# Performance work log

Measured on AMD Instinct MI355X. Metric: run time of the kernel, lower is better.

## Reference

```python
import jax, jax.numpy as jnp
import numpy as np

B, L, D_MODEL = 2, 2048, 1024
N_HEADS, D_K = 16, 64  # d_v == d_k (required by the output*q epilogue)


def setup_inputs() -> dict:
    key = jax.random.key(0)
    ks = jax.random.split(key, 8)
    # xavier_normal std for [d_model, d_k] fan: sqrt(2/(d_model+d_k))
    std = float(np.sqrt(2.0 / (D_MODEL + D_K)))
    std_p = float(np.sqrt(1.0 / (N_HEADS * D_K)))  # nn.Linear default ~ U(-1/sqrt(fan_in),..); normal approx ok for a baseline
    return {
        "q": jax.random.normal(ks[0], (B, L, D_MODEL), jnp.float32),
        "k": jax.random.normal(ks[1], (B, L, D_MODEL), jnp.float32),
        "v": jax.random.normal(ks[2], (B, L, D_MODEL), jnp.float32),
        "w_qs": jax.random.normal(ks[3], (N_HEADS, D_MODEL, D_K), jnp.float32) * std,
        "w_ks": jax.random.normal(ks[4], (N_HEADS, D_MODEL, D_K), jnp.float32) * std,
        "w_vs": jax.random.normal(ks[5], (N_HEADS, D_MODEL, D_K), jnp.float32) * std,
        "w_proj": jax.random.normal(ks[6], (D_MODEL, N_HEADS * D_K), jnp.float32) * std_p,
        "b_proj": jnp.zeros((D_MODEL,), jnp.float32),
    }


def reference(q, k, v, w_qs, w_ks, w_vs, w_proj, b_proj):
    # Per-head projections: [h, B, L, d_k]
    qh = jnp.einsum("bld,hdk->hblk", q, w_qs)
    kh = jnp.einsum("bld,hdk->hblk", k, w_ks)
    vh = jnp.einsum("bld,hdk->hblk", v, w_vs)
    # UNscaled attention (no 1/sqrt(d_k)), dropout is identity at eval
    attn = jax.nn.softmax(jnp.einsum("hblk,hbmk->hblm", qh, kh), axis=-1)
    # attn @ V with elementwise *q epilogue
    out = jnp.einsum("hblm,hbmk->hblk", attn, vh) * qh
    # torch.cat(torch.split(outputs, mb_size, 0), -1): heads concat on last dim
    out = out.transpose(1, 2, 0, 3).reshape(q.shape[0], q.shape[1], -1)  # [B, L, h*d_k]
    return out @ w_proj.T + b_proj
```

## Files before the change

### kernel.cpp

```cpp
#include <hip/hip_runtime.h>

#define B_ 2
#define L_ 2048
#define DM 1024
#define H_ 16
#define DK 64
#define ROWS (B_*L_)
#define BK 32
#define LDT 40

typedef _Float16 f16x8 __attribute__((ext_vector_type(8)));
typedef float    f32x4 __attribute__((ext_vector_type(4)));
typedef unsigned short us8 __attribute__((ext_vector_type(8)));
typedef unsigned short us4v __attribute__((ext_vector_type(4)));

__device__ __forceinline__ unsigned short f2h(float f) {
    _Float16 h = (_Float16)f;
    return __builtin_bit_cast(unsigned short, h);
}
__device__ __forceinline__ float h2f(unsigned short u) {
    return (float)__builtin_bit_cast(_Float16, u);
}
__device__ __forceinline__ f16x8 ld8h(const unsigned short* p) {
    return *reinterpret_cast<const f16x8*>(p);
}
__device__ __forceinline__ us8 cvt_us8(float4 a, float4 b) {
    us8 u;
    u[0] = f2h(a.x); u[1] = f2h(a.y); u[2] = f2h(a.z); u[3] = f2h(a.w);
    u[4] = f2h(b.x); u[5] = f2h(b.y); u[6] = f2h(b.z); u[7] = f2h(b.w);
    return u;
}

#define MFMA(a, b, c) __builtin_amdgcn_mfma_f32_16x16x32_f16((a), (b), (c), 0, 0, 0)

#define AS1 __attribute__((address_space(1)))
#define AS3 __attribute__((address_space(3)))
__device__ __forceinline__ void glds16(const void* g, void* l) {
    __builtin_amdgcn_global_load_lds((const AS1 unsigned int*)g,
                                     (AS3 unsigned int*)l, 16, 0, 0);
}

__global__ __launch_bounds__(256) void kcvt(
    const float* __restrict__ src, unsigned short* __restrict__ dst)
{
    size_t i = ((size_t)blockIdx.x * 256 + threadIdx.x) * 8;
    const float4* s4 = (const float4*)(src + i);
    *(us8*)(dst + i) = cvt_us8(s4[0], s4[1]);
}

__global__ __launch_bounds__(256) void kcvt3(
    const float* __restrict__ q, const float* __restrict__ k,
    const float* __restrict__ v, unsigned short* __restrict__ dst)
{
    int bx = blockIdx.x;
    int which = bx >> 11, rem = bx & 2047;
    const float* src = (which == 0) ? q : (which == 1) ? k : v;
    size_t i = ((size_t)rem * 256 + threadIdx.x) * 8;
    const float4* s4 = (const float4*)(src + i);
    *(us8*)(dst + (size_t)which * ROWS * DM + i) = cvt_us8(s4[0], s4[1]);
}

__global__ __launch_bounds__(256) void k0_transpose_w(
    const float* __restrict__ wq,
    const float* __restrict__ wk,
    const float* __restrict__ wv,
    unsigned short* __restrict__ wt)
{
    __shared__ unsigned short tile[64][65];
    int bx = blockIdx.x;
    int which = bx / (H_ * 16);
    int rem   = bx % (H_ * 16);
    int h  = rem >> 4;
    int db = (rem & 15) * 64;
    const float* src = (which == 0) ? wq : (which == 1) ? wk : wv;
    float scale = (which == 1) ? 1.44269504f : 1.0f;

    int t = threadIdx.x;
    int r = t >> 2;
    int c = (t & 3) * 16;
    const float4* sp = (const float4*)(src + ((size_t)(h * DM + db + r)) * DK + c);
    #pragma unroll
    for (int i4 = 0; i4 < 4; i4++) {
        float4 f = sp[i4];
        tile[r][c + i4 * 4 + 0] = f2h(f.x * scale);
        tile[r][c + i4 * 4 + 1] = f2h(f.y * scale);
        tile[r][c + i4 * 4 + 2] = f2h(f.z * scale);
        tile[r][c + i4 * 4 + 3] = f2h(f.w * scale);
    }
    __syncthreads();

    int n   = t >> 2;
    int d16 = (t & 3) * 16;
    __align__(16) unsigned short ov[16];
    #pragma unroll
    for (int i = 0; i < 16; i++) ov[i] = tile[d16 + i][n];
    size_t off = (((size_t)which * H_ + h) * DK + n) * DM + db + d16;
    *(us8*)(wt + off)     = *(us8*)&ov[0];
    *(us8*)(wt + off + 8) = *(us8*)&ov[8];
}

__global__ __launch_bounds__(256) void k1_proj_fp16(
    const unsigned short* __restrict__ qkvh,
    const unsigned short* __restrict__ wt,
    unsigned short* __restrict__ qh,
    unsigned short* __restrict__ kh,
    unsigned short* __restrict__ vt)
{
    __shared__ __align__(16) unsigned short sA[128 * BK];
    __shared__ __align__(16) unsigned short sB[128 * BK];

    int bx = blockIdx.x;
    int which = bx >> 8;
    int rem   = bx & 255;
    int mbase = (rem >> 3) * 128;
    int nbase = (rem & 7) * 128;

    const unsigned short* Ag = qkvh + (size_t)which * ROWS * DM;
    const unsigned short* Bg = wt + (size_t)which * DM * DM;

    int t = threadIdx.x;
    int wave = t >> 6, lane = t & 63, quad = lane >> 4, l16 = lane & 15;
    int wm = (wave >> 1) * 64, wn = (wave & 1) * 64;

    const unsigned short* gA0 = Ag + (size_t)(mbase + (t >> 2)) * DM + (t & 3) * 8;
    const unsigned short* gA1 = gA0 + (size_t)64 * DM;
    const unsigned short* gB0 = Bg + (size_t)(nbase + (t >> 2)) * DM + (t & 3) * 8;
    const unsigned short* gB1 = gB0 + (size_t)64 * DM;
    unsigned short* lA0 = &sA[(size_t)t * 8];
    unsigned short* lA1 = &sA[(size_t)(256 + t) * 8];
    unsigned short* lB0 = &sB[(size_t)t * 8];
    unsigned short* lB1 = &sB[(size_t)(256 + t) * 8];

    f32x4 acc[4][4];
    #pragma unroll
    for (int mi = 0; mi < 4; mi++)
        #pragma unroll
        for (int ni = 0; ni < 4; ni++) acc[mi][ni] = (f32x4)0.0f;

    for (int step = 0; step < 32; step++) {
        if (step) __syncthreads();
        glds16(gA0, lA0); glds16(gA1, lA1);
        glds16(gB0, lB0); glds16(gB1, lB1);
        gA0 += BK; gA1 += BK; gB0 += BK; gB1 += BK;
        __syncthreads();

        f16x8 aF[4], bF[4];
        #pragma unroll
        for (int mi = 0; mi < 4; mi++)
            aF[mi] = *(const f16x8*)&sA[(wm + mi * 16 + l16) * BK + quad * 8];
        #pragma unroll
        for (int ni = 0; ni < 4; ni++)
            bF[ni] = *(const f16x8*)&sB[(wn + ni * 16 + l16) * BK + quad * 8];
        __builtin_amdgcn_s_setprio(1);
        #pragma unroll
        for (int mi = 0; mi < 4; mi++)
            #pragma unroll
            for (int ni = 0; ni < 4; ni++)
                acc[mi][ni] = MFMA(aF[mi], bF[ni], acc[mi][ni]);
        __builtin_amdgcn_s_setprio(0);
    }

    int h = (nbase >> 6) + (wave & 1);
    if (which < 2) {
        unsigned short* OUT = ((which == 0) ? qh : kh) + (size_t)h * ROWS * DK;
        #pragma unroll
        for (int mi = 0; mi < 4; mi++)
            #pragma unroll
            for (int ni = 0; ni < 4; ni++)
                #pragma unroll
                for (int r = 0; r < 4; r++) {
                    int row = mbase + wm + mi * 16 + quad * 4 + r;
                    OUT[(size_t)row * DK + ni * 16 + l16] = f2h(acc[mi][ni][r]);
                }
    } else {
        unsigned short* OUT = vt + (size_t)h * DK * ROWS;
        #pragma unroll
        for (int mi = 0; mi < 4; mi++)
            #pragma unroll
            for (int ni = 0; ni < 4; ni++) {
                int dk   = ni * 16 + l16;
                int rowb = mbase + wm + mi * 16 + quad * 4;
                us4v pk;
                pk[0] = f2h(acc[mi][ni][0]); pk[1] = f2h(acc[mi][ni][1]);
                pk[2] = f2h(acc[mi][ni][2]); pk[3] = f2h(acc[mi][ni][3]);
                *(us4v*)(OUT + (size_t)dk * ROWS + rowb) = pk;
            }
    }
}

__global__ __launch_bounds__(256) void k1_proj_qkv(
    const float* __restrict__ q,
    const float* __restrict__ k,
    const float* __restrict__ v,
    const unsigned short* __restrict__ wt,
    unsigned short* __restrict__ qh,
    unsigned short* __restrict__ kh,
    unsigned short* __restrict__ vt)
{
    __shared__ __align__(16) unsigned short sA[128 * LDT];
    __shared__ __align__(16) unsigned short sB[128 * LDT];

    int bx = blockIdx.x;
    int which = bx >> 8;
    int rem   = bx & 255;
    int mbase = (rem >> 3) * 128;
    int nbase = (rem & 7) * 128;

    const float* Ag = (which == 0) ? q : (which == 1) ? k : v;
    const unsigned short* Bg = wt + (size_t)which * DM * DM;

    int t = threadIdx.x;
    int wave = t >> 6, lane = t & 63, quad = lane >> 4, l16 = lane & 15;
    int wm = (wave >> 1) * 64, wn = (wave & 1) * 64;

    int ar0 = t >> 2,         ac0 = t & 3;
    int ar1 = (256 + t) >> 2, ac1 = t & 3;
    const float* pA0 = Ag + (size_t)(mbase + ar0) * DM + ac0 * 8;
    const float* pA1 = Ag + (size_t)(mbase + ar1) * DM + ac1 * 8;
    const unsigned short* pB0 = Bg + (size_t)(nbase + ar0) * DM + ac0 * 8;
    const unsigned short* pB1 = Bg + (size_t)(nbase + ar1) * DM + ac1 * 8;
    unsigned short* wA0 = &sA[ar0 * LDT + ac0 * 8];
    unsigned short* wA1 = &sA[ar1 * LDT + ac1 * 8];
    unsigned short* wB0 = &sB[ar0 * LDT + ac0 * 8];
    unsigned short* wB1 = &sB[ar1 * LDT + ac1 * 8];

    f32x4 acc[4][4];
    #pragma unroll
    for (int mi = 0; mi < 4; mi++)
        #pragma unroll
        for (int ni = 0; ni < 4; ni++) acc[mi][ni] = (f32x4)0.0f;

    float4 rA0a = *(const float4*)pA0, rA0b = *(const float4*)(pA0 + 4);
    float4 rA1a = *(const float4*)pA1, rA1b = *(const float4*)(pA1 + 4);
    us8 rB0 = *(const us8*)pB0, rB1 = *(const us8*)pB1;

    for (int step = 0; step < 32; step++) {
        if (step) __syncthreads();
        *(us8*)wA0 = cvt_us8(rA0a, rA0b);
        *(us8*)wA1 = cvt_us8(rA1a, rA1b);
        *(us8*)wB0 = rB0; *(us8*)wB1 = rB1;
        __syncthreads();
        if (step < 31) {
            pA0 += BK; pA1 += BK; pB0 += BK; pB1 += BK;
            rA0a = *(const float4*)pA0; rA0b = *(const float4*)(pA0 + 4);
            rA1a = *(const float4*)pA1; rA1b = *(const float4*)(pA1 + 4);
            rB0 = *(const us8*)pB0; rB1 = *(const us8*)pB1;
        }
        f16x8 aF[4], bF[4];
        #pragma unroll
        for (int mi = 0; mi < 4; mi++)
            aF[mi] = *(const f16x8*)&sA[(wm + mi * 16 + l16) * LDT + quad * 8];
        #pragma unroll
        for (int ni = 0; ni < 4; ni++)
            bF[ni] = *(const f16x8*)&sB[(wn + ni * 16 + l16) * LDT + quad * 8];
        #pragma unroll
        for (int mi = 0; mi < 4; mi++)
            #pragma unroll
            for (int ni = 0; ni < 4; ni++)
                acc[mi][ni] = MFMA(aF[mi], bF[ni], acc[mi][ni]);
    }

    int h = (nbase >> 6) + (wave & 1);
    if (which < 2) {
        unsigned short* OUT = ((which == 0) ? qh : kh) + (size_t)h * ROWS * DK;
        #pragma unroll
        for (int mi = 0; mi < 4; mi++)
            #pragma unroll
            for (int ni = 0; ni < 4; ni++)
                #pragma unroll
                for (int r = 0; r < 4; r++) {
                    int row = mbase + wm + mi * 16 + quad * 4 + r;
                    OUT[(size_t)row * DK + ni * 16 + l16] = f2h(acc[mi][ni][r]);
                }
    } else {
        unsigned short* OUT = vt + (size_t)h * DK * ROWS;
        #pragma unroll
        for (int mi = 0; mi < 4; mi++)
            #pragma unroll
            for (int ni = 0; ni < 4; ni++) {
                int dk   = ni * 16 + l16;
                int rowb = mbase + wm + mi * 16 + quad * 4;
                us4v pk;
                pk[0] = f2h(acc[mi][ni][0]); pk[1] = f2h(acc[mi][ni][1]);
                pk[2] = f2h(acc[mi][ni][2]); pk[3] = f2h(acc[mi][ni][3]);
                *(us4v*)(OUT + (size_t)dk * ROWS + rowb) = pk;
            }
    }
}

__global__ __launch_bounds__(256) void k2_attn(
    const unsigned short* __restrict__ qh,
    const unsigned short* __restrict__ kh,
    const unsigned short* __restrict__ vt,
    unsigned short* __restrict__ x2)
{
    __shared__ __align__(16) unsigned short ktile[2][64][64];
    __shared__ __align__(16) unsigned short vtile[2][64][64];
    __shared__ __align__(16) unsigned short pld[4][16][64];

    int bx = blockIdx.x;
    int xcd = bx & 7;
    int loc = bx >> 3;
    int hb  = xcd * 4 + (loc >> 5);
    int qt  = loc & 31;
    int h = hb >> 1, b = hb & 1;
    int qbase = qt * 64;

    const unsigned short* qhp = qh + ((size_t)h * ROWS + b * L_) * DK;
    const unsigned short* khp = kh + ((size_t)h * ROWS + b * L_) * DK;
    const unsigned short* vtp = vt + (size_t)h * DK * ROWS + b * L_;

    int wave = threadIdx.x >> 6, lane = threadIdx.x & 63;
    int quad = lane >> 4, l16 = lane & 15;
    int t = threadIdx.x;
    int g8 = (l16 & 7) * 8;

    int c0 = t,       key0 = c0 >> 3, ss0 = ((c0 & 7) ^ (key0 & 7)) * 8;
    int c1 = 256 + t, key1 = c1 >> 3, ss1 = ((c1 & 7) ^ (key1 & 7)) * 8;
    const unsigned short* kg0 = khp + (size_t)key0 * DK + ss0;
    const unsigned short* kg1 = khp + (size_t)key1 * DK + ss1;
    const unsigned short* vg0 = vtp + (size_t)key0 * ROWS + ss0;
    const unsigned short* vg1 = vtp + (size_t)key1 * ROWS + ss1;
    unsigned short* kl0[2] = { &ktile[0][0][0] + c0 * 8, &ktile[1][0][0] + c0 * 8 };
    unsigned short* kl1[2] = { &ktile[0][0][0] + c1 * 8, &ktile[1][0][0] + c1 * 8 };
    unsigned short* vl0[2] = { &vtile[0][0][0] + c0 * 8, &vtile[1][0][0] + c0 * 8 };
    unsigned short* vl1[2] = { &vtile[0][0][0] + c1 * 8, &vtile[1][0][0] + c1 * 8 };

    const unsigned short* kgp0 = kg0 + (size_t)2 * 64 * DK;
    const unsigned short* kgp1 = kg1 + (size_t)2 * 64 * DK;
    const unsigned short* vgp0 = vg0 + 64;
    const unsigned short* vgp1 = vg1 + 64;

    glds16(kg0, kl0[0]); glds16(kg1, kl1[0]);
    glds16(kg0 + (size_t)64 * DK, kl0[1]); glds16(kg1 + (size_t)64 * DK, kl1[1]);
    glds16(vg0, vl0[0]); glds16(vg1, vl1[0]);

    int qrow = qbase + wave * 16 + l16;
    f16x8 qb0 = ld8h(qhp + (size_t)qrow * DK + quad * 8);
    f16x8 qb1 = ld8h(qhp + (size_t)qrow * DK + 32 + quad * 8);

    float m_i = -1e30f, l_i = 0.0f;
    f32x4 o[4];
    #pragma unroll
    for (int nt = 0; nt < 4; nt++) o[nt] = (f32x4)0.0f;

    f32x4 s0[4], s1[4];

    __syncthreads();

    #pragma unroll
    for (int nt = 0; nt < 4; nt++) s0[nt] = (f32x4)0.0f;
    __builtin_amdgcn_s_setprio(1);
    #pragma unroll
    for (int nt = 0; nt < 4; nt++) {
        const unsigned short* kr = &ktile[0][nt * 16 + l16][0];
        f16x8 ka0 = *(const f16x8*)(kr + ((quad * 8) ^ g8));
        f16x8 ka1 = *(const f16x8*)(kr + ((32 + quad * 8) ^ g8));
        s0[nt] = MFMA(ka0, qb0, s0[nt]);
        s0[nt] = MFMA(ka1, qb1, s0[nt]);
    }
    __builtin_amdgcn_s_setprio(0);
    __syncthreads();

#define K2_BODY(SP, SN, KT, CUR)                                              \
    {                                                                         \
        if ((KT) < 31) {                                                      \
            _Pragma("unroll")                                                 \
            for (int nt = 0; nt < 4; nt++) SN[nt] = (f32x4)0.0f;              \
            __builtin_amdgcn_s_setprio(1);                                    \
            _Pragma("unroll")                                                 \
            for (int nt = 0; nt < 4; nt++) {                                  \
                const unsigned short* kr = &ktile[(CUR)^1][nt * 16 + l16][0]; \
                f16x8 ka0 = *(const f16x8*)(kr + ((quad * 8) ^ g8));          \
                f16x8 ka1 = *(const f16x8*)(kr + ((32 + quad * 8) ^ g8));     \
                SN[nt] = MFMA(ka0, qb0, SN[nt]);                              \
                SN[nt] = MFMA(ka1, qb1, SN[nt]);                              \
            }                                                                 \
            __builtin_amdgcn_s_setprio(0);                                    \
        }                                                                     \
        if ((KT) < 30) {                                                      \
            glds16(kgp0, kl0[CUR]); glds16(kgp1, kl1[CUR]);                   \
            kgp0 += (size_t)64 * DK; kgp1 += (size_t)64 * DK;                 \
        }                                                                     \
        if ((KT) < 31) {                                                      \
            glds16(vgp0, vl0[(CUR)^1]); glds16(vgp1, vl1[(CUR)^1]);           \
            vgp0 += 64; vgp1 += 64;                                           \
        }                                                                     \
                                                 \
        float pm[4];                                                          \
        _Pragma("unroll")                                                     \
        for (int nt = 0; nt < 4; nt++) {                                      \
            float a = fmaxf(SP[nt][0], SP[nt][1]);                            \
            float c2 = fmaxf(SP[nt][2], SP[nt][3]);                           \
            pm[nt] = fmaxf(a, c2);                                            \
        }                                                                     \
        float mx = fmaxf(fmaxf(pm[0], pm[1]), fmaxf(pm[2], pm[3]));           \
        mx = fmaxf(mx, __shfl_xor(mx, 16));                                   \
        mx = fmaxf(mx, __shfl_xor(mx, 32));                                   \
        if (!__all(mx - m_i <= 11.0f)) {                                      \
            float mnew  = fmaxf(m_i, mx);                                     \
            float alpha = __builtin_amdgcn_exp2f(m_i - mnew);                 \
            l_i *= alpha;                                                     \
            _Pragma("unroll")                                                 \
            for (int r = 0; r < 4; r++) {                                     \
                float av = __shfl(alpha, quad * 4 + r);                       \
                _Pragma("unroll")                                             \
                for (int nt = 0; nt < 4; nt++) o[nt][r] *= av;                \
            }                                                                 \
            m_i = mnew;                                                       \
        }                                                                     \
        float ps[4];                                                          \
        _Pragma("unroll")                                                     \
        for (int nt = 0; nt < 4; nt++) {                                      \
            float e0 = __builtin_amdgcn_exp2f(SP[nt][0] - m_i);               \
            float e1 = __builtin_amdgcn_exp2f(SP[nt][1] - m_i);               \
            float e2 = __builtin_amdgcn_exp2f(SP[nt][2] - m_i);               \
            float e3 = __builtin_amdgcn_exp2f(SP[nt][3] - m_i);               \
            SP[nt][0] = e0; SP[nt][1] = e1; SP[nt][2] = e2; SP[nt][3] = e3;   \
            ps[nt] = (e0 + e1) + (e2 + e3);                                   \
        }                                                                     \
        float rs = (ps[0] + ps[1]) + (ps[2] + ps[3]);                         \
        rs += __shfl_xor(rs, 16);                                             \
        rs += __shfl_xor(rs, 32);                                             \
        l_i += rs;                                                            \
        _Pragma("unroll")                                                     \
        for (int nt = 0; nt < 4; nt++) {                                      \
            us4v pk;                                                          \
            pk[0] = f2h(SP[nt][0]); pk[1] = f2h(SP[nt][1]);                   \
            pk[2] = f2h(SP[nt][2]); pk[3] = f2h(SP[nt][3]);                   \
            *(us4v*)&pld[wave][l16][(nt * 16 + quad * 4) ^ g8] = pk;          \
        }                                                                     \
                                                      \
        __builtin_amdgcn_s_setprio(1);                                        \
        _Pragma("unroll")                                                     \
        for (int kk = 0; kk < 2; kk++) {                                      \
            f16x8 pa = *(const f16x8*)&pld[wave][l16][(kk*32 + quad*8) ^ g8]; \
            _Pragma("unroll")                                                 \
            for (int nt = 0; nt < 4; nt++) {                                  \
                const unsigned short* vr = &vtile[CUR][nt * 16 + l16][0];     \
                f16x8 vb = *(const f16x8*)(vr + ((kk * 32 + quad * 8) ^ g8)); \
                o[nt] = MFMA(pa, vb, o[nt]);                                  \
            }                                                                 \
        }                                                                     \
        __builtin_amdgcn_s_setprio(0);                                        \
        __syncthreads();                                                      \
    }

    for (int kt = 0; kt < 32; kt += 2) {
        K2_BODY(s0, s1, kt,     0)
        K2_BODY(s1, s0, kt + 1, 1)
    }
#undef K2_BODY

    float linv = 1.0f / l_i;
    #pragma unroll
    for (int r = 0; r < 4; r++) {
        float lv = __shfl(linv, quad * 4 + r);
        int row = qbase + wave * 16 + quad * 4 + r;
        #pragma unroll
        for (int nt = 0; nt < 4; nt++) {
            int col = nt * 16 + l16;
            float qv = h2f(qhp[(size_t)row * DK + col]);
            float val = o[nt][r] * lv * qv;
            x2[((size_t)b * L_ + row) * DM + h * DK + col] = f2h(val);
        }
    }
}

__global__ __launch_bounds__(256) void k3_out_proj(
    const unsigned short* __restrict__ x2,
    const unsigned short* __restrict__ wph,
    const float* __restrict__ bias,
    float* __restrict__ out)
{
    __shared__ __align__(16) unsigned short sA[128 * BK];
    __shared__ __align__(16) unsigned short sB[128 * BK];

    int bx = blockIdx.x;
    int mbase = (bx >> 3) * 128;
    int nbase = (bx & 7) * 128;

    int t = threadIdx.x;
    int wave = t >> 6, lane = t & 63, quad = lane >> 4, l16 = lane & 15;
    int wm = (wave >> 1) * 64, wn = (wave & 1) * 64;

    const unsigned short* gA0 = x2 + (size_t)(mbase + (t >> 2)) * DM + (t & 3) * 8;
    const unsigned short* gA1 = gA0 + (size_t)64 * DM;
    const unsigned short* gB0 = wph + (size_t)(nbase + (t >> 2)) * DM + (t & 3) * 8;
    const unsigned short* gB1 = gB0 + (size_t)64 * DM;
    unsigned short* lA0 = &sA[(size_t)t * 8];
    unsigned short* lA1 = &sA[(size_t)(256 + t) * 8];
    unsigned short* lB0 = &sB[(size_t)t * 8];
    unsigned short* lB1 = &sB[(size_t)(256 + t) * 8];

    f32x4 acc[4][4];
    #pragma unroll
    for (int mi = 0; mi < 4; mi++)
        #pragma unroll
        for (int ni = 0; ni < 4; ni++) acc[mi][ni] = (f32x4)0.0f;

    for (int step = 0; step < 32; step++) {
        if (step) __syncthreads();
        glds16(gA0, lA0); glds16(gA1, lA1);
        glds16(gB0, lB0); glds16(gB1, lB1);
        gA0 += BK; gA1 += BK; gB0 += BK; gB1 += BK;
        __syncthreads();

        f16x8 aF[4], bF[4];
        #pragma unroll
        for (int mi = 0; mi < 4; mi++)
            aF[mi] = *(const f16x8*)&sA[(wm + mi * 16 + l16) * BK + quad * 8];
        #pragma unroll
        for (int ni = 0; ni < 4; ni++)
            bF[ni] = *(const f16x8*)&sB[(wn + ni * 16 + l16) * BK + quad * 8];
        __builtin_amdgcn_s_setprio(1);
        #pragma unroll
        for (int mi = 0; mi < 4; mi++)
            #pragma unroll
            for (int ni = 0; ni < 4; ni++)
                acc[mi][ni] = MFMA(aF[mi], bF[ni], acc[mi][ni]);
        __builtin_amdgcn_s_setprio(0);
    }

    float bv[4];
    #pragma unroll
    for (int ni = 0; ni < 4; ni++) bv[ni] = bias[nbase + wn + ni * 16 + l16];

    #pragma unroll
    for (int mi = 0; mi < 4; mi++)
        #pragma unroll
        for (int ni = 0; ni < 4; ni++)
            #pragma unroll
            for (int r = 0; r < 4; r++) {
                int row = mbase + wm + mi * 16 + quad * 4 + r;
                int col = nbase + wn + ni * 16 + l16;
                out[(size_t)row * DM + col] = acc[mi][ni][r] + bv[ni];
            }
}

extern "C" void kernel_launch(void* const* d_in, const int* in_sizes, int n_in,
                              void* d_out, int out_size, void* d_ws, size_t ws_size,
                              hipStream_t stream)
{
    const float* q     = (const float*)d_in[0];
    const float* k     = (const float*)d_in[1];
    const float* v     = (const float*)d_in[2];
    const float* wqs   = (const float*)d_in[3];
    const float* wks   = (const float*)d_in[4];
    const float* wvs   = (const float*)d_in[5];
    const float* wproj = (const float*)d_in[6];
    const float* bproj = (const float*)d_in[7];
    float* out = (float*)d_out;

    char* ws = (char*)d_ws;
    #define MB (size_t)(1024 * 1024)
    unsigned short* wt   = (unsigned short*)(ws);
    unsigned short* wph  = (unsigned short*)(ws + 6  * MB);
    unsigned short* qh   = (unsigned short*)(ws + 8  * MB);
    unsigned short* kh   = (unsigned short*)(ws + 16 * MB);
    unsigned short* vt   = (unsigned short*)(ws + 24 * MB);
    unsigned short* x2   = (unsigned short*)(ws + 32 * MB);
    unsigned short* qkvh = (unsigned short*)(ws + 32 * MB);

    kcvt<<<dim3((DM * DM) / (256 * 8)), dim3(256), 0, stream>>>(wproj, wph);
    k0_transpose_w<<<dim3(3 * H_ * 16), dim3(256), 0, stream>>>(wqs, wks, wvs, wt);

    if (ws_size >= 56 * MB) {
        kcvt3<<<dim3(3 * 2048), dim3(256), 0, stream>>>(q, k, v, qkvh);
        k1_proj_fp16<<<dim3(3 * 32 * 8), dim3(256), 0, stream>>>(qkvh, wt, qh, kh, vt);
    } else {
        k1_proj_qkv<<<dim3(3 * 32 * 8), dim3(256), 0, stream>>>(q, k, v, wt, qh, kh, vt);
    }
    k2_attn<<<dim3(H_ * B_ * 32), dim3(256), 0, stream>>>(qh, kh, vt, x2);
    k3_out_proj<<<dim3(32 * 8), dim3(256), 0, stream>>>(x2, wph, bproj, out);
}
```

Before: 254.8 us.

## Fuse fp32 input conversion into projection GEMM, swizzle LDS, restructure attention pipeline

Removes the separate fp32-to-fp16 conversion pass over q, k, v and has the projection GEMM load fp32 tiles into LDS directly via global_load_lds, converting to fp16 when it reads the fragments. This saves a full read and write of the activations, at the cost of twice the LDS traffic and conversion work inside the loop. Both GEMMs also get XOR-swizzled LDS layouts to avoid bank conflicts and a block-index remap for better L2 locality. The attention loop changes from computing the next tile's scores ahead to a simpler single-step double buffer, and switches to packed cvt_pkrtz for P.

```diff
diff --git a/kernel.cpp b/kernel.cpp
--- a/kernel.cpp
+++ b/kernel.cpp
@@ -7,9 +7,10 @@
 #define DK 64
 #define ROWS (B_*L_)
 #define BK 32
-#define LDT 40
 
 typedef _Float16 f16x8 __attribute__((ext_vector_type(8)));
+typedef __fp16   fp16v2 __attribute__((ext_vector_type(2)));
+typedef __fp16   fp16v4 __attribute__((ext_vector_type(4)));
 typedef float    f32x4 __attribute__((ext_vector_type(4)));
 typedef unsigned short us8 __attribute__((ext_vector_type(8)));
 typedef unsigned short us4v __attribute__((ext_vector_type(4)));
@@ -46,18 +47,6 @@
     size_t i = ((size_t)blockIdx.x * 256 + threadIdx.x) * 8;
     const float4* s4 = (const float4*)(src + i);
     *(us8*)(dst + i) = cvt_us8(s4[0], s4[1]);
-}
-
-__global__ __launch_bounds__(256) void kcvt3(
-    const float* __restrict__ q, const float* __restrict__ k,
-    const float* __restrict__ v, unsigned short* __restrict__ dst)
-{
-    int bx = blockIdx.x;
-    int which = bx >> 11, rem = bx & 2047;
-    const float* src = (which == 0) ? q : (which == 1) ? k : v;
-    size_t i = ((size_t)rem * 256 + threadIdx.x) * 8;
-    const float4* s4 = (const float4*)(src + i);
-    *(us8*)(dst + (size_t)which * ROWS * DM + i) = cvt_us8(s4[0], s4[1]);
 }
 
 __global__ __launch_bounds__(256) void k0_transpose_w(
@@ -99,37 +88,50 @@
     *(us8*)(wt + off + 8) = *(us8*)&ov[8];
 }
 
-__global__ __launch_bounds__(256) void k1_proj_fp16(
-    const unsigned short* __restrict__ qkvh,
+__global__ __launch_bounds__(256) void k1_proj(
+    const float* __restrict__ q,
+    const float* __restrict__ k,
+    const float* __restrict__ v,
     const unsigned short* __restrict__ wt,
     unsigned short* __restrict__ qh,
     unsigned short* __restrict__ kh,
     unsigned short* __restrict__ vt)
 {
-    __shared__ __align__(16) unsigned short sA[128 * BK];
-    __shared__ __align__(16) unsigned short sB[128 * BK];
-
-    int bx = blockIdx.x;
+    __shared__ __align__(16) float          sAf[128 * 32];
+    __shared__ __align__(16) unsigned short sB [128 * 32];
+
+    int bxr = blockIdx.x;
+    int bx  = (bxr & 7) * 96 + (bxr >> 3);
     int which = bx >> 8;
     int rem   = bx & 255;
     int mbase = (rem >> 3) * 128;
     int nbase = (rem & 7) * 128;
 
-    const unsigned short* Ag = qkvh + (size_t)which * ROWS * DM;
+    const float* Ag = (which == 0) ? q : (which == 1) ? k : v;
     const unsigned short* Bg = wt + (size_t)which * DM * DM;
 
     int t = threadIdx.x;
     int wave = t >> 6, lane = t & 63, quad = lane >> 4, l16 = lane & 15;
     int wm = (wave >> 1) * 64, wn = (wave & 1) * 64;
-
-    const unsigned short* gA0 = Ag + (size_t)(mbase + (t >> 2)) * DM + (t & 3) * 8;
-    const unsigned short* gA1 = gA0 + (size_t)64 * DM;
-    const unsigned short* gB0 = Bg + (size_t)(nbase + (t >> 2)) * DM + (t & 3) * 8;
-    const unsigned short* gB1 = gB0 + (size_t)64 * DM;
-    unsigned short* lA0 = &sA[(size_t)t * 8];
-    unsigned short* lA1 = &sA[(size_t)(256 + t) * 8];
-    unsigned short* lB0 = &sB[(size_t)t * 8];
-    unsigned short* lB1 = &sB[(size_t)(256 + t) * 8];
+    int xa = l16 & 7;
+    int xb = (l16 >> 1) & 3;
+
+    const float* gA[4]; float* lA[4];
+    #pragma unroll
+    for (int i = 0; i < 4; i++) {
+        int c = i * 256 + t;
+        int row = c >> 3, sl = (c & 7) ^ (row & 7);
+        gA[i] = Ag + (size_t)(mbase + row) * DM + sl * 4;
+        lA[i] = sAf + c * 4;
+    }
+    const unsigned short* gB[2]; unsigned short* lB[2];
+    #pragma unroll
+    for (int i = 0; i < 2; i++) {
+        int c = i * 256 + t;
+        int row = c >> 2, sl = (c & 3) ^ ((row >> 1) & 3);
+        gB[i] = Bg + (size_t)(nbase + row) * DM + sl * 8;
+        lB[i] = sB + c * 8;
+    }
 
     f32x4 acc[4][4];
     #pragma unroll
@@ -139,18 +141,31 @@
 
     for (int step = 0; step < 32; step++) {
         if (step) __syncthreads();
-        glds16(gA0, lA0); glds16(gA1, lA1);
-        glds16(gB0, lB0); glds16(gB1, lB1);
-        gA0 += BK; gA1 += BK; gB0 += BK; gB1 += BK;
+        glds16(gA[0], lA[0]); glds16(gA[1], lA[1]);
+        glds16(gA[2], lA[2]); glds16(gA[3], lA[3]);
+        glds16(gB[0], lB[0]); glds16(gB[1], lB[1]);
+        #pragma unroll
+        for (int i = 0; i < 4; i++) gA[i] += BK;
+        gB[0] += BK; gB[1] += BK;
         __syncthreads();
 
         f16x8 aF[4], bF[4];
         #pragma unroll
-        for (int mi = 0; mi < 4; mi++)
-            aF[mi] = *(const f16x8*)&sA[(wm + mi * 16 + l16) * BK + quad * 8];
+        for (int mi = 0; mi < 4; mi++) {
+            const float* ar = sAf + (wm + mi * 16 + l16) * 32;
+            f32x4 a0 = *(const f32x4*)(ar + (((quad * 2)     ^ xa) * 4));
+            f32x4 a1 = *(const f32x4*)(ar + (((quad * 2 + 1) ^ xa) * 4));
+            f16x8 af;
+            af[0] = (_Float16)a0[0]; af[1] = (_Float16)a0[1];
+            af[2] = (_Float16)a0[2]; af[3] = (_Float16)a0[3];
+            af[4] = (_Float16)a1[0]; af[5] = (_Float16)a1[1];
+            af[6] = (_Float16)a1[2]; af[7] = (_Float16)a1[3];
+            aF[mi] = af;
+        }
         #pragma unroll
         for (int ni = 0; ni < 4; ni++)
-            bF[ni] = *(const f16x8*)&sB[(wn + ni * 16 + l16) * BK + quad * 8];
+            bF[ni] = *(const f16x8*)(sB + (wn + ni * 16 + l16) * 32
+                                        + ((quad ^ xb) * 8));
         __builtin_amdgcn_s_setprio(1);
         #pragma unroll
         for (int mi = 0; mi < 4; mi++)
@@ -188,106 +203,6 @@
     }
 }
 
-__global__ __launch_bounds__(256) void k1_proj_qkv(
-    const float* __restrict__ q,
-    const float* __restrict__ k,
-    const float* __restrict__ v,
-    const unsigned short* __restrict__ wt,
-    unsigned short* __restrict__ qh,
-    unsigned short* __restrict__ kh,
-    unsigned short* __restrict__ vt)
-{
-    __shared__ __align__(16) unsigned short sA[128 * LDT];
-    __shared__ __align__(16) unsigned short sB[128 * LDT];
-
-    int bx = blockIdx.x;
-    int which = bx >> 8;
-    int rem   = bx & 255;
-    int mbase = (rem >> 3) * 128;
-    int nbase = (rem & 7) * 128;
-
-    const float* Ag = (which == 0) ? q : (which == 1) ? k : v;
-    const unsigned short* Bg = wt + (size_t)which * DM * DM;
-
-    int t = threadIdx.x;
-    int wave = t >> 6, lane = t & 63, quad = lane >> 4, l16 = lane & 15;
-    int wm = (wave >> 1) * 64, wn = (wave & 1) * 64;
-
-    int ar0 = t >> 2,         ac0 = t & 3;
-    int ar1 = (256 + t) >> 2, ac1 = t & 3;
-    const float* pA0 = Ag + (size_t)(mbase + ar0) * DM + ac0 * 8;
-    const float* pA1 = Ag + (size_t)(mbase + ar1) * DM + ac1 * 8;
-    const unsigned short* pB0 = Bg + (size_t)(nbase + ar0) * DM + ac0 * 8;
-    const unsigned short* pB1 = Bg + (size_t)(nbase + ar1) * DM + ac1 * 8;
-    unsigned short* wA0 = &sA[ar0 * LDT + ac0 * 8];
-    unsigned short* wA1 = &sA[ar1 * LDT + ac1 * 8];
-    unsigned short* wB0 = &sB[ar0 * LDT + ac0 * 8];
-    unsigned short* wB1 = &sB[ar1 * LDT + ac1 * 8];
-
-    f32x4 acc[4][4];
-    #pragma unroll
-    for (int mi = 0; mi < 4; mi++)
-        #pragma unroll
-        for (int ni = 0; ni < 4; ni++) acc[mi][ni] = (f32x4)0.0f;
-
-    float4 rA0a = *(const float4*)pA0, rA0b = *(const float4*)(pA0 + 4);
-    float4 rA1a = *(const float4*)pA1, rA1b = *(const float4*)(pA1 + 4);
-    us8 rB0 = *(const us8*)pB0, rB1 = *(const us8*)pB1;
-
-    for (int step = 0; step < 32; step++) {
-        if (step) __syncthreads();
-        *(us8*)wA0 = cvt_us8(rA0a, rA0b);
-        *(us8*)wA1 = cvt_us8(rA1a, rA1b);
-        *(us8*)wB0 = rB0; *(us8*)wB1 = rB1;
-        __syncthreads();
-        if (step < 31) {
-            pA0 += BK; pA1 += BK; pB0 += BK; pB1 += BK;
-            rA0a = *(const float4*)pA0; rA0b = *(const float4*)(pA0 + 4);
-            rA1a = *(const float4*)pA1; rA1b = *(const float4*)(pA1 + 4);
-            rB0 = *(const us8*)pB0; rB1 = *(const us8*)pB1;
-        }
-        f16x8 aF[4], bF[4];
-        #pragma unroll
-        for (int mi = 0; mi < 4; mi++)
-            aF[mi] = *(const f16x8*)&sA[(wm + mi * 16 + l16) * LDT + quad * 8];
-        #pragma unroll
-        for (int ni = 0; ni < 4; ni++)
-            bF[ni] = *(const f16x8*)&sB[(wn + ni * 16 + l16) * LDT + quad * 8];
-        #pragma unroll
-        for (int mi = 0; mi < 4; mi++)
-            #pragma unroll
-            for (int ni = 0; ni < 4; ni++)
-                acc[mi][ni] = MFMA(aF[mi], bF[ni], acc[mi][ni]);
-    }
-
-    int h = (nbase >> 6) + (wave & 1);
-    if (which < 2) {
-        unsigned short* OUT = ((which == 0) ? qh : kh) + (size_t)h * ROWS * DK;
-        #pragma unroll
-        for (int mi = 0; mi < 4; mi++)
-            #pragma unroll
-            for (int ni = 0; ni < 4; ni++)
-                #pragma unroll
-                for (int r = 0; r < 4; r++) {
-                    int row = mbase + wm + mi * 16 + quad * 4 + r;
-                    OUT[(size_t)row * DK + ni * 16 + l16] = f2h(acc[mi][ni][r]);
-                }
-    } else {
-        unsigned short* OUT = vt + (size_t)h * DK * ROWS;
-        #pragma unroll
-        for (int mi = 0; mi < 4; mi++)
-            #pragma unroll
-            for (int ni = 0; ni < 4; ni++) {
-                int dk   = ni * 16 + l16;
-                int rowb = mbase + wm + mi * 16 + quad * 4;
-                us4v pk;
-                pk[0] = f2h(acc[mi][ni][0]); pk[1] = f2h(acc[mi][ni][1]);
-                pk[2] = f2h(acc[mi][ni][2]); pk[3] = f2h(acc[mi][ni][3]);
-                *(us4v*)(OUT + (size_t)dk * ROWS + rowb) = pk;
-            }
-    }
-}
-
 __global__ __launch_bounds__(256) void k2_attn(
     const unsigned short* __restrict__ qh,
     const unsigned short* __restrict__ kh,
@@ -326,13 +241,7 @@
     unsigned short* vl0[2] = { &vtile[0][0][0] + c0 * 8, &vtile[1][0][0] + c0 * 8 };
     unsigned short* vl1[2] = { &vtile[0][0][0] + c1 * 8, &vtile[1][0][0] + c1 * 8 };
 
-    const unsigned short* kgp0 = kg0 + (size_t)2 * 64 * DK;
-    const unsigned short* kgp1 = kg1 + (size_t)2 * 64 * DK;
-    const unsigned short* vgp0 = vg0 + 64;
-    const unsigned short* vgp1 = vg1 + 64;
-
     glds16(kg0, kl0[0]); glds16(kg1, kl1[0]);
-    glds16(kg0 + (size_t)64 * DK, kl0[1]); glds16(kg1 + (size_t)64 * DK, kl1[1]);
     glds16(vg0, vl0[0]); glds16(vg1, vl1[0]);
 
     int qrow = qbase + wave * 16 + l16;
@@ -344,54 +253,34 @@
     #pragma unroll
     for (int nt = 0; nt < 4; nt++) o[nt] = (f32x4)0.0f;
 
-    f32x4 s0[4], s1[4];
-
     __syncthreads();
 
-    #pragma unroll
-    for (int nt = 0; nt < 4; nt++) s0[nt] = (f32x4)0.0f;
-    __builtin_amdgcn_s_setprio(1);
-    #pragma unroll
-    for (int nt = 0; nt < 4; nt++) {
-        const unsigned short* kr = &ktile[0][nt * 16 + l16][0];
-        f16x8 ka0 = *(const f16x8*)(kr + ((quad * 8) ^ g8));
-        f16x8 ka1 = *(const f16x8*)(kr + ((32 + quad * 8) ^ g8));
-        s0[nt] = MFMA(ka0, qb0, s0[nt]);
-        s0[nt] = MFMA(ka1, qb1, s0[nt]);
-    }
-    __builtin_amdgcn_s_setprio(0);
-    __syncthreads();
-
-#define K2_BODY(SP, SN, KT, CUR)                                              \
+#define K2_STEP(KT, CUR)                                                      \
     {                                                                         \
         if ((KT) < 31) {                                                      \
-            _Pragma("unroll")                                                 \
-            for (int nt = 0; nt < 4; nt++) SN[nt] = (f32x4)0.0f;              \
-            __builtin_amdgcn_s_setprio(1);                                    \
-            _Pragma("unroll")                                                 \
-            for (int nt = 0; nt < 4; nt++) {                                  \
-                const unsigned short* kr = &ktile[(CUR)^1][nt * 16 + l16][0]; \
-                f16x8 ka0 = *(const f16x8*)(kr + ((quad * 8) ^ g8));          \
-                f16x8 ka1 = *(const f16x8*)(kr + ((32 + quad * 8) ^ g8));     \
-                SN[nt] = MFMA(ka0, qb0, SN[nt]);                              \
-                SN[nt] = MFMA(ka1, qb1, SN[nt]);                              \
-            }                                                                 \
-            __builtin_amdgcn_s_setprio(0);                                    \
-        }                                                                     \
-        if ((KT) < 30) {                                                      \
-            glds16(kgp0, kl0[CUR]); glds16(kgp1, kl1[CUR]);                   \
-            kgp0 += (size_t)64 * DK; kgp1 += (size_t)64 * DK;                 \
-        }                                                                     \
-        if ((KT) < 31) {                                                      \
-            glds16(vgp0, vl0[(CUR)^1]); glds16(vgp1, vl1[(CUR)^1]);           \
-            vgp0 += 64; vgp1 += 64;                                           \
-        }                                                                     \
-                                                 \
+            size_t ko = (size_t)((KT) + 1) * 64 * DK;                         \
+            size_t vo = (size_t)((KT) + 1) * 64;                              \
+            glds16(kg0 + ko, kl0[(CUR) ^ 1]); glds16(kg1 + ko, kl1[(CUR) ^ 1]);\
+            glds16(vg0 + vo, vl0[(CUR) ^ 1]); glds16(vg1 + vo, vl1[(CUR) ^ 1]);\
+        }                                                                     \
+        f32x4 s[4];                                                           \
+        _Pragma("unroll")                                                     \
+        for (int nt = 0; nt < 4; nt++) s[nt] = (f32x4)0.0f;                   \
+        __builtin_amdgcn_s_setprio(1);                                        \
+        _Pragma("unroll")                                                     \
+        for (int nt = 0; nt < 4; nt++) {                                      \
+            const unsigned short* kr = &ktile[CUR][nt * 16 + l16][0];         \
+            f16x8 ka0 = *(const f16x8*)(kr + ((quad * 8) ^ g8));              \
+            f16x8 ka1 = *(const f16x8*)(kr + ((32 + quad * 8) ^ g8));         \
+            s[nt] = MFMA(ka0, qb0, s[nt]);                                    \
+            s[nt] = MFMA(ka1, qb1, s[nt]);                                    \
+        }                                                                     \
+        __builtin_amdgcn_s_setprio(0);                                        \
         float pm[4];                                                          \
         _Pragma("unroll")                                                     \
         for (int nt = 0; nt < 4; nt++) {                                      \
-            float a = fmaxf(SP[nt][0], SP[nt][1]);                            \
-            float c2 = fmaxf(SP[nt][2], SP[nt][3]);                           \
+            float a = fmaxf(s[nt][0], s[nt][1]);                              \
+            float c2 = fmaxf(s[nt][2], s[nt][3]);                             \
             pm[nt] = fmaxf(a, c2);                                            \
         }                                                                     \
         float mx = fmaxf(fmaxf(pm[0], pm[1]), fmaxf(pm[2], pm[3]));           \
@@ -412,11 +301,11 @@
         float ps[4];                                                          \
         _Pragma("unroll")                                                     \
         for (int nt = 0; nt < 4; nt++) {                                      \
-            float e0 = __builtin_amdgcn_exp2f(SP[nt][0] - m_i);               \
-            float e1 = __builtin_amdgcn_exp2f(SP[nt][1] - m_i);               \
-            float e2 = __builtin_amdgcn_exp2f(SP[nt][2] - m_i);               \
-            float e3 = __builtin_amdgcn_exp2f(SP[nt][3] - m_i);               \
-            SP[nt][0] = e0; SP[nt][1] = e1; SP[nt][2] = e2; SP[nt][3] = e3;   \
+            float e0 = __builtin_amdgcn_exp2f(s[nt][0] - m_i);                \
+            float e1 = __builtin_amdgcn_exp2f(s[nt][1] - m_i);                \
+            float e2 = __builtin_amdgcn_exp2f(s[nt][2] - m_i);                \
+            float e3 = __builtin_amdgcn_exp2f(s[nt][3] - m_i);                \
+            s[nt][0] = e0; s[nt][1] = e1; s[nt][2] = e2; s[nt][3] = e3;       \
             ps[nt] = (e0 + e1) + (e2 + e3);                                   \
         }                                                                     \
         float rs = (ps[0] + ps[1]) + (ps[2] + ps[3]);                         \
@@ -425,16 +314,15 @@
         l_i += rs;                                                            \
         _Pragma("unroll")                                                     \
         for (int nt = 0; nt < 4; nt++) {                                      \
-            us4v pk;                                                          \
-            pk[0] = f2h(SP[nt][0]); pk[1] = f2h(SP[nt][1]);                   \
-            pk[2] = f2h(SP[nt][2]); pk[3] = f2h(SP[nt][3]);                   \
-            *(us4v*)&pld[wave][l16][(nt * 16 + quad * 4) ^ g8] = pk;          \
-        }                                                                     \
-                                                      \
+            fp16v2 p01 = __builtin_amdgcn_cvt_pkrtz(s[nt][0], s[nt][1]);      \
+            fp16v2 p23 = __builtin_amdgcn_cvt_pkrtz(s[nt][2], s[nt][3]);      \
+            fp16v4 pk4 = __builtin_shufflevector(p01, p23, 0, 1, 2, 3);       \
+            *(fp16v4*)&pld[wave][l16][(nt * 16 + quad * 4) ^ g8] = pk4;       \
+        }                                                                     \
         __builtin_amdgcn_s_setprio(1);                                        \
         _Pragma("unroll")                                                     \
         for (int kk = 0; kk < 2; kk++) {                                      \
-            f16x8 pa = *(const f16x8*)&pld[wave][l16][(kk*32 + quad*8) ^ g8]; \
+            f16x8 pa = *(const f16x8*)&pld[wave][l16][(kk * 32 + quad * 8) ^ g8];\
             _Pragma("unroll")                                                 \
             for (int nt = 0; nt < 4; nt++) {                                  \
                 const unsigned short* vr = &vtile[CUR][nt * 16 + l16][0];     \
@@ -446,11 +334,11 @@
         __syncthreads();                                                      \
     }
 
-    for (int kt = 0; kt < 32; kt += 2) {
-        K2_BODY(s0, s1, kt,     0)
-        K2_BODY(s1, s0, kt + 1, 1)
-    }
-#undef K2_BODY
+    for (int kt2 = 0; kt2 < 32; kt2 += 2) {
+        K2_STEP(kt2,     0)
+        K2_STEP(kt2 + 1, 1)
+    }
+#undef K2_STEP
 
     float linv = 1.0f / l_i;
     #pragma unroll
@@ -476,22 +364,27 @@
     __shared__ __align__(16) unsigned short sA[128 * BK];
     __shared__ __align__(16) unsigned short sB[128 * BK];
 
-    int bx = blockIdx.x;
+    int bxr = blockIdx.x;
+    int bx  = (bxr & 7) * 32 + (bxr >> 3);
     int mbase = (bx >> 3) * 128;
     int nbase = (bx & 7) * 128;
 
     int t = threadIdx.x;
     int wave = t >> 6, lane = t & 63, quad = lane >> 4, l16 = lane & 15;
     int wm = (wave >> 1) * 64, wn = (wave & 1) * 64;
-
-    const unsigned short* gA0 = x2 + (size_t)(mbase + (t >> 2)) * DM + (t & 3) * 8;
-    const unsigned short* gA1 = gA0 + (size_t)64 * DM;
-    const unsigned short* gB0 = wph + (size_t)(nbase + (t >> 2)) * DM + (t & 3) * 8;
-    const unsigned short* gB1 = gB0 + (size_t)64 * DM;
-    unsigned short* lA0 = &sA[(size_t)t * 8];
-    unsigned short* lA1 = &sA[(size_t)(256 + t) * 8];
-    unsigned short* lB0 = &sB[(size_t)t * 8];
-    unsigned short* lB1 = &sB[(size_t)(256 + t) * 8];
+    int xb = (l16 >> 1) & 3;
+
+    const unsigned short* gA[2]; unsigned short* lA[2];
+    const unsigned short* gB[2]; unsigned short* lB[2];
+    #pragma unroll
+    for (int i = 0; i < 2; i++) {
+        int c = i * 256 + t;
+        int row = c >> 2, sl = (c & 3) ^ ((row >> 1) & 3);
+        gA[i] = x2  + (size_t)(mbase + row) * DM + sl * 8;
+        gB[i] = wph + (size_t)(nbase + row) * DM + sl * 8;
+        lA[i] = sA + c * 8;
+        lB[i] = sB + c * 8;
+    }
 
     f32x4 acc[4][4];
     #pragma unroll
@@ -501,18 +394,20 @@
 
     for (int step = 0; step < 32; step++) {
         if (step) __syncthreads();
-        glds16(gA0, lA0); glds16(gA1, lA1);
-        glds16(gB0, lB0); glds16(gB1, lB1);
-        gA0 += BK; gA1 += BK; gB0 += BK; gB1 += BK;
+        glds16(gA[0], lA[0]); glds16(gA[1], lA[1]);
+        glds16(gB[0], lB[0]); glds16(gB[1], lB[1]);
+        gA[0] += BK; gA[1] += BK; gB[0] += BK; gB[1] += BK;
         __syncthreads();
 
         f16x8 aF[4], bF[4];
         #pragma unroll
         for (int mi = 0; mi < 4; mi++)
-            aF[mi] = *(const f16x8*)&sA[(wm + mi * 16 + l16) * BK + quad * 8];
+            aF[mi] = *(const f16x8*)(sA + (wm + mi * 16 + l16) * BK
+                                        + ((quad ^ xb) * 8));
         #pragma unroll
         for (int ni = 0; ni < 4; ni++)
-            bF[ni] = *(const f16x8*)&sB[(wn + ni * 16 + l16) * BK + quad * 8];
+            bF[ni] = *(const f16x8*)(sB + (wn + ni * 16 + l16) * BK
+                                        + ((quad ^ xb) * 8));
         __builtin_amdgcn_s_setprio(1);
         #pragma unroll
         for (int mi = 0; mi < 4; mi++)
@@ -560,17 +455,10 @@
     unsigned short* kh   = (unsigned short*)(ws + 16 * MB);
     unsigned short* vt   = (unsigned short*)(ws + 24 * MB);
     unsigned short* x2   = (unsigned short*)(ws + 32 * MB);
-    unsigned short* qkvh = (unsigned short*)(ws + 32 * MB);
 
     kcvt<<<dim3((DM * DM) / (256 * 8)), dim3(256), 0, stream>>>(wproj, wph);
     k0_transpose_w<<<dim3(3 * H_ * 16), dim3(256), 0, stream>>>(wqs, wks, wvs, wt);
-
-    if (ws_size >= 56 * MB) {
-        kcvt3<<<dim3(3 * 2048), dim3(256), 0, stream>>>(q, k, v, qkvh);
-        k1_proj_fp16<<<dim3(3 * 32 * 8), dim3(256), 0, stream>>>(qkvh, wt, qh, kh, vt);
-    } else {
-        k1_proj_qkv<<<dim3(3 * 32 * 8), dim3(256), 0, stream>>>(q, k, v, wt, qh, kh, vt);
-    }
+    k1_proj<<<dim3(3 * 32 * 8), dim3(256), 0, stream>>>(q, k, v, wt, qh, kh, vt);
     k2_attn<<<dim3(H_ * B_ * 32), dim3(256), 0, stream>>>(qh, kh, vt, x2);
     k3_out_proj<<<dim3(32 * 8), dim3(256), 0, stream>>>(x2, wph, bproj, out);
 }
```

New measurement: 247.5 us. 1.03x faster.
